# Kernel tuning notes

Hardware: AMD Instinct MI355X
Metric: run time of the kernel (lower is better)

The kernel has to match this reference:

```python
import jax, jax.numpy as jnp
import numpy as np

EPS = 1e-8  # torch.nn.CosineSimilarity default eps


def setup_inputs() -> dict:
    key = jax.random.key(0)
    k1, k2 = jax.random.split(key)
    action_set = jax.random.normal(k1, (1_000_000, 64), dtype=jnp.float32)
    pred_action = jax.random.normal(k2, (32, 4, 64), dtype=jnp.float32)
    return {"pred_action": pred_action, "action_set": action_set}


def reference(pred_action, action_set):
    # pred_action: [B, T, D] (a 2-D [B, D] input would be unsqueezed to T=1)
    # action_set:  [N, D]
    if pred_action.ndim == 2:
        pred_action = pred_action[:, None, :]
    # torch CosineSimilarity: x1.x2 / max(||x1|| * ||x2||, eps)
    dot = jnp.einsum('nd,btd->nbt', action_set, pred_action)        # [N, B, T]
    na = jnp.linalg.norm(action_set, axis=-1)                       # [N]
    nb = jnp.linalg.norm(pred_action, axis=-1)                      # [B, T]
    sims = dot / jnp.maximum(na[:, None, None] * nb[None, :, :], EPS)
    amax = jnp.argmax(sims, axis=0)                                  # [B, T]
    return action_set[amax]                                          # [B, T, D]
```

## Files before the change

### kernel.cpp

```cpp
#include <hip/hip_runtime.h>
#include <hip/hip_bf16.h>
#include <math.h>

#define D        64
#define NQ       128
#define TS       64
#define MARGIN   0.025f
#define CAP      128

typedef __attribute__((ext_vector_type(8))) short  short8;
typedef __attribute__((ext_vector_type(4))) float  f32x4;

__device__ inline unsigned ordf(float f) {
    unsigned u = __float_as_uint(f);
    return (u & 0x80000000u) ? ~u : (u | 0x80000000u);
}

__device__ inline short bf16bits(float f) {
    __hip_bfloat16 h = __float2bfloat16(f);
    return *(short*)&h;
}

__device__ inline float sq16(f32x4 a, f32x4 b, f32x4 c, f32x4 d) {
    float s = 0.f;
    s = fmaf(a.x, a.x, s); s = fmaf(a.y, a.y, s); s = fmaf(a.z, a.z, s); s = fmaf(a.w, a.w, s);
    s = fmaf(b.x, b.x, s); s = fmaf(b.y, b.y, s); s = fmaf(b.z, b.z, s); s = fmaf(b.w, b.w, s);
    s = fmaf(c.x, c.x, s); s = fmaf(c.y, c.y, s); s = fmaf(c.z, c.z, s); s = fmaf(c.w, c.w, s);
    s = fmaf(d.x, d.x, s); s = fmaf(d.y, d.y, s); s = fmaf(d.z, d.z, s); s = fmaf(d.w, d.w, s);
    return s;
}

__device__ inline short8 cvt8(f32x4 a, f32x4 b, float s) {
    short8 r;
    r[0] = bf16bits(a.x * s); r[1] = bf16bits(a.y * s);
    r[2] = bf16bits(a.z * s); r[3] = bf16bits(a.w * s);
    r[4] = bf16bits(b.x * s); r[5] = bf16bits(b.y * s);
    r[6] = bf16bits(b.z * s); r[7] = bf16bits(b.w * s);
    return r;
}

__global__ __launch_bounds__(256, 2)
void k1_score(const float* __restrict__ pred,
              const float* __restrict__ acts,
              float* __restrict__ tmax,
              int ntiles)
{
    const int tid  = threadIdx.x;
    const int lane = tid & 63;
    const int quad = lane >> 4;
    const int l15  = lane & 15;
    const int wid  = blockIdx.x * 4 + (tid >> 6);
    const int nw   = gridDim.x * 4;

    short8 bf[8][2];
#pragma unroll
    for (int nt = 0; nt < 8; ++nt) {
        const int q = nt * 16 + l15;
        const float* P = pred + q * D + quad * 8;
        f32x4 v0 = *(const f32x4*)(P);
        f32x4 v1 = *(const f32x4*)(P + 4);
        f32x4 v2 = *(const f32x4*)(P + 32);
        f32x4 v3 = *(const f32x4*)(P + 36);
        float nb2 = sq16(v0, v1, v2, v3);
        nb2 += __shfl_xor(nb2, 16);
        nb2 += __shfl_xor(nb2, 32);
        const float rnb = 1.0f / sqrtf(nb2);
        bf[nt][0] = cvt8(v0, v1, rnb);
        bf[nt][1] = cvt8(v2, v3, rnb);
    }

    for (int tile = wid; tile < ntiles; tile += nw) {
        const float* base = acts + (size_t)tile * (TS * D);

        f32x4 af[4][2][2];
#pragma unroll
        for (int mt = 0; mt < 4; ++mt) {
            const float* rp = base + (mt * 16 + l15) * D + quad * 8;
#pragma unroll
            for (int ks = 0; ks < 2; ++ks) {
                af[mt][ks][0] = *(const f32x4*)(rp + ks * 32);
                af[mt][ks][1] = *(const f32x4*)(rp + ks * 32 + 4);
            }
        }

        short8 abf[4][2];
#pragma unroll
        for (int mt = 0; mt < 4; ++mt) {
            float s = sq16(af[mt][0][0], af[mt][0][1], af[mt][1][0], af[mt][1][1]);
            s += __shfl_xor(s, 16);
            s += __shfl_xor(s, 32);
            const float r = 1.0f / sqrtf(s);
            abf[mt][0] = cvt8(af[mt][0][0], af[mt][0][1], r);
            abf[mt][1] = cvt8(af[mt][1][0], af[mt][1][1], r);
        }

#pragma unroll
        for (int nt = 0; nt < 8; ++nt) {
            f32x4 acc[4];
#pragma unroll
            for (int mt = 0; mt < 4; ++mt) acc[mt] = (f32x4){0.f, 0.f, 0.f, 0.f};
#pragma unroll
            for (int ks = 0; ks < 2; ++ks)
#pragma unroll
                for (int mt = 0; mt < 4; ++mt)
                    acc[mt] = __builtin_amdgcn_mfma_f32_16x16x32_bf16(
                        abf[mt][ks], bf[nt][ks], acc[mt], 0, 0, 0);

            float m = -3.0e38f;
#pragma unroll
            for (int mt = 0; mt < 4; ++mt) {
                m = fmaxf(m, fmaxf(fmaxf(acc[mt].x, acc[mt].y),
                                   fmaxf(acc[mt].z, acc[mt].w)));
            }
            m = fmaxf(m, __shfl_xor(m, 16));
            m = fmaxf(m, __shfl_xor(m, 32));
            if (quad == 0)
                tmax[(size_t)(nt * 16 + l15) * ntiles + tile] = m;
        }
    }
}

__global__ __launch_bounds__(256, 2)
void k2_rescore(const float* __restrict__ pred,
                const float* __restrict__ acts,
                const float* __restrict__ tmax,
                float* __restrict__ out,
                int ntiles)
{
    __shared__ float wmax[4];
    __shared__ int   cnt;
    __shared__ int   list[CAP];

    const int q   = blockIdx.x;
    const int tid = threadIdx.x;
    const float* row = tmax + (size_t)q * ntiles;

    if (tid == 0) cnt = 0;
    float m = -3.0e38f;
    for (int t = tid; t < ntiles; t += 256) m = fmaxf(m, row[t]);
#pragma unroll
    for (int off = 1; off < 64; off <<= 1) m = fmaxf(m, __shfl_xor(m, off));
    if ((tid & 63) == 0) wmax[tid >> 6] = m;
    __syncthreads();
    m = fmaxf(fmaxf(wmax[0], wmax[1]), fmaxf(wmax[2], wmax[3]));
    const float thr = m - MARGIN;

    for (int t = tid; t < ntiles; t += 256) {
        if (row[t] >= thr) {
            int i = atomicAdd(&cnt, 1);
            if (i < CAP) list[i] = t;
        }
    }
    __syncthreads();
    const int n = min(cnt, CAP);

    if (tid < 64) {
        const f32x4* P = (const f32x4*)(pred + q * D);
        unsigned long long best = 0ull;
        for (int i = 0; i < n; ++i) {
            const int r = list[i] * TS + tid;
            const f32x4* A = (const f32x4*)(acts + (size_t)r * D);
            float dot = 0.f, na2 = 0.f;
#pragma unroll
            for (int c = 0; c < 16; ++c) {
                f32x4 a = A[c];
                f32x4 p = P[c];
                dot = fmaf(a.x, p.x, dot); na2 = fmaf(a.x, a.x, na2);
                dot = fmaf(a.y, p.y, dot); na2 = fmaf(a.y, a.y, na2);
                dot = fmaf(a.z, p.z, dot); na2 = fmaf(a.z, a.z, na2);
                dot = fmaf(a.w, p.w, dot); na2 = fmaf(a.w, a.w, na2);
            }
            float sim = dot * (1.0f / sqrtf(na2));
            unsigned long long key =
                ((unsigned long long)ordf(sim) << 32) | (unsigned)(~r);
#pragma unroll
            for (int off = 1; off < 64; off <<= 1) {
                unsigned long long o = __shfl_xor(key, off);
                if (o > key) key = o;
            }
            if (key > best) best = key;
        }
        const unsigned idx = ~(unsigned)(best & 0xffffffffull);
        out[q * D + tid] = acts[(size_t)idx * D + tid];
    }
}

extern "C" void kernel_launch(void* const* d_in, const int* in_sizes, int n_in,
                              void* d_out, int out_size, void* d_ws, size_t ws_size,
                              hipStream_t stream)
{
    const float* pred = (const float*)d_in[0];
    const float* acts = (const float*)d_in[1];
    long n0 = in_sizes[0], n1 = in_sizes[1];
    if (n0 > n1) {
        const float* t = pred; pred = acts; acts = t;
        long tt = n0; n0 = n1; n1 = tt;
    }
    const int N      = (int)(n1 / D);
    const int ntiles = N / TS;

    float* tmax = (float*)d_ws;
    float* out  = (float*)d_out;

    k1_score<<<dim3(512), dim3(256), 0, stream>>>(pred, acts, tmax, ntiles);
    k2_rescore<<<dim3(NQ), dim3(256), 0, stream>>>(pred, acts, tmax, out, ntiles);
}
```

Measured before the change: 392.8 us.

## Stage action tiles in double-buffered LDS shared across waves with query split

Each block now loads a 64-row action tile cooperatively with coalesced loads, normalizes it, and converts it to bf16 into a padded, double-buffered LDS array. The four waves each handle 32 of the 128 queries against the shared tile, and the next tile's global load is prefetched while the current tile's MFMAs run. This replaces the old scheme where each wave loaded and converted its own tile and held all 128 query fragments in registers. The aim is better load coalescing, less redundant conversion and fewer registers, which allows 3 blocks per SM and a 768-block grid. The cost is a __syncthreads per tile and LDS traffic.

```diff
diff --git a/kernel.cpp b/kernel.cpp
--- a/kernel.cpp
+++ b/kernel.cpp
@@ -5,10 +5,12 @@
 #define D        64
 #define NQ       128
 #define TS       64
+#define ASTRIDE  72
 #define MARGIN   0.025f
 #define CAP      128
 
 typedef __attribute__((ext_vector_type(8))) short  short8;
+typedef __attribute__((ext_vector_type(4))) short  short4v;
 typedef __attribute__((ext_vector_type(4))) float  f32x4;
 
 __device__ inline unsigned ordf(float f) {
@@ -21,13 +23,15 @@
     return *(short*)&h;
 }
 
+__device__ inline float sq4(f32x4 a) {
+    float s = 0.f;
+    s = fmaf(a.x, a.x, s); s = fmaf(a.y, a.y, s);
+    s = fmaf(a.z, a.z, s); s = fmaf(a.w, a.w, s);
+    return s;
+}
+
 __device__ inline float sq16(f32x4 a, f32x4 b, f32x4 c, f32x4 d) {
-    float s = 0.f;
-    s = fmaf(a.x, a.x, s); s = fmaf(a.y, a.y, s); s = fmaf(a.z, a.z, s); s = fmaf(a.w, a.w, s);
-    s = fmaf(b.x, b.x, s); s = fmaf(b.y, b.y, s); s = fmaf(b.z, b.z, s); s = fmaf(b.w, b.w, s);
-    s = fmaf(c.x, c.x, s); s = fmaf(c.y, c.y, s); s = fmaf(c.z, c.z, s); s = fmaf(c.w, c.w, s);
-    s = fmaf(d.x, d.x, s); s = fmaf(d.y, d.y, s); s = fmaf(d.z, d.z, s); s = fmaf(d.w, d.w, s);
-    return s;
+    return sq4(a) + sq4(b) + sq4(c) + sq4(d);
 }
 
 __device__ inline short8 cvt8(f32x4 a, f32x4 b, float s) {
@@ -39,23 +43,31 @@
     return r;
 }
 
-__global__ __launch_bounds__(256, 2)
+__device__ inline short4v cvt4(f32x4 a, float s) {
+    short4v r;
+    r[0] = bf16bits(a.x * s); r[1] = bf16bits(a.y * s);
+    r[2] = bf16bits(a.z * s); r[3] = bf16bits(a.w * s);
+    return r;
+}
+
+__global__ __launch_bounds__(256, 3)
 void k1_score(const float* __restrict__ pred,
               const float* __restrict__ acts,
               float* __restrict__ tmax,
               int ntiles)
 {
+    __shared__ unsigned short As[2][TS * ASTRIDE];
+
     const int tid  = threadIdx.x;
     const int lane = tid & 63;
+    const int wv   = tid >> 6;
     const int quad = lane >> 4;
     const int l15  = lane & 15;
-    const int wid  = blockIdx.x * 4 + (tid >> 6);
-    const int nw   = gridDim.x * 4;
-
-    short8 bf[8][2];
-#pragma unroll
-    for (int nt = 0; nt < 8; ++nt) {
-        const int q = nt * 16 + l15;
+
+    short8 bf[2][2];
+#pragma unroll
+    for (int nt = 0; nt < 2; ++nt) {
+        const int q = (wv * 2 + nt) * 16 + l15;
         const float* P = pred + q * D + quad * 8;
         f32x4 v0 = *(const f32x4*)(P);
         f32x4 v1 = *(const f32x4*)(P + 4);
@@ -69,54 +81,89 @@
         bf[nt][1] = cvt8(v2, v3, rnb);
     }
 
-    for (int tile = wid; tile < ntiles; tile += nw) {
-        const float* base = acts + (size_t)tile * (TS * D);
-
-        f32x4 af[4][2][2];
-#pragma unroll
-        for (int mt = 0; mt < 4; ++mt) {
-            const float* rp = base + (mt * 16 + l15) * D + quad * 8;
-#pragma unroll
-            for (int ks = 0; ks < 2; ++ks) {
-                af[mt][ks][0] = *(const f32x4*)(rp + ks * 32);
-                af[mt][ks][1] = *(const f32x4*)(rp + ks * 32 + 4);
-            }
-        }
-
-        short8 abf[4][2];
-#pragma unroll
-        for (int mt = 0; mt < 4; ++mt) {
-            float s = sq16(af[mt][0][0], af[mt][0][1], af[mt][1][0], af[mt][1][1]);
-            s += __shfl_xor(s, 16);
-            s += __shfl_xor(s, 32);
-            const float r = 1.0f / sqrtf(s);
-            abf[mt][0] = cvt8(af[mt][0][0], af[mt][0][1], r);
-            abf[mt][1] = cvt8(af[mt][1][0], af[mt][1][1], r);
-        }
-
-#pragma unroll
-        for (int nt = 0; nt < 8; ++nt) {
-            f32x4 acc[4];
-#pragma unroll
-            for (int mt = 0; mt < 4; ++mt) acc[mt] = (f32x4){0.f, 0.f, 0.f, 0.f};
+    int tile = blockIdx.x;
+    if (tile >= ntiles) return;
+
+    {
+        const f32x4* src = (const f32x4*)(acts + (size_t)tile * (TS * D));
+        f32x4 v[4];
+#pragma unroll
+        for (int i = 0; i < 4; ++i) v[i] = src[tid + i * 256];
+#pragma unroll
+        for (int i = 0; i < 4; ++i) {
+            const int c   = tid + i * 256;
+            const int row = c >> 4, col = c & 15;
+            float s = sq4(v[i]);
+            s += __shfl_xor(s, 1); s += __shfl_xor(s, 2);
+            s += __shfl_xor(s, 4); s += __shfl_xor(s, 8);
+            *(short4v*)&As[0][row * ASTRIDE + col * 4] = cvt4(v[i], 1.0f / sqrtf(s));
+        }
+    }
+    __syncthreads();
+
+    int p = 0;
+    while (true) {
+        const int tn = tile + gridDim.x;
+        const bool have_next = tn < ntiles;
+
+        f32x4 v[4];
+        if (have_next) {
+            const f32x4* src = (const f32x4*)(acts + (size_t)tn * (TS * D));
+#pragma unroll
+            for (int i = 0; i < 4; ++i) v[i] = src[tid + i * 256];
+        }
+
+        short8 af[4][2];
+#pragma unroll
+        for (int mt = 0; mt < 4; ++mt)
 #pragma unroll
             for (int ks = 0; ks < 2; ++ks)
+                af[mt][ks] = *(const short8*)
+                    &As[p][(mt * 16 + l15) * ASTRIDE + ks * 32 + quad * 8];
+
+        f32x4 acc[2][4];
+#pragma unroll
+        for (int nt = 0; nt < 2; ++nt)
+#pragma unroll
+            for (int mt = 0; mt < 4; ++mt) acc[nt][mt] = (f32x4){0.f, 0.f, 0.f, 0.f};
+#pragma unroll
+        for (int ks = 0; ks < 2; ++ks)
+#pragma unroll
+            for (int nt = 0; nt < 2; ++nt)
 #pragma unroll
                 for (int mt = 0; mt < 4; ++mt)
-                    acc[mt] = __builtin_amdgcn_mfma_f32_16x16x32_bf16(
-                        abf[mt][ks], bf[nt][ks], acc[mt], 0, 0, 0);
-
+                    acc[nt][mt] = __builtin_amdgcn_mfma_f32_16x16x32_bf16(
+                        af[mt][ks], bf[nt][ks], acc[nt][mt], 0, 0, 0);
+
+#pragma unroll
+        for (int nt = 0; nt < 2; ++nt) {
             float m = -3.0e38f;
 #pragma unroll
-            for (int mt = 0; mt < 4; ++mt) {
-                m = fmaxf(m, fmaxf(fmaxf(acc[mt].x, acc[mt].y),
-                                   fmaxf(acc[mt].z, acc[mt].w)));
-            }
+            for (int mt = 0; mt < 4; ++mt)
+                m = fmaxf(m, fmaxf(fmaxf(acc[nt][mt].x, acc[nt][mt].y),
+                                   fmaxf(acc[nt][mt].z, acc[nt][mt].w)));
             m = fmaxf(m, __shfl_xor(m, 16));
             m = fmaxf(m, __shfl_xor(m, 32));
-            if (quad == 0)
-                tmax[(size_t)(nt * 16 + l15) * ntiles + tile] = m;
-        }
+            if (quad == 0) {
+                const int q = (wv * 2 + nt) * 16 + l15;
+                tmax[(size_t)q * ntiles + tile] = m;
+            }
+        }
+
+        if (!have_next) break;
+
+#pragma unroll
+        for (int i = 0; i < 4; ++i) {
+            const int c   = tid + i * 256;
+            const int row = c >> 4, col = c & 15;
+            float s = sq4(v[i]);
+            s += __shfl_xor(s, 1); s += __shfl_xor(s, 2);
+            s += __shfl_xor(s, 4); s += __shfl_xor(s, 8);
+            *(short4v*)&As[p ^ 1][row * ASTRIDE + col * 4] = cvt4(v[i], 1.0f / sqrtf(s));
+        }
+        __syncthreads();
+        p ^= 1;
+        tile = tn;
     }
 }
 
@@ -164,11 +211,11 @@
 #pragma unroll
             for (int c = 0; c < 16; ++c) {
                 f32x4 a = A[c];
-                f32x4 p = P[c];
-                dot = fmaf(a.x, p.x, dot); na2 = fmaf(a.x, a.x, na2);
-                dot = fmaf(a.y, p.y, dot); na2 = fmaf(a.y, a.y, na2);
-                dot = fmaf(a.z, p.z, dot); na2 = fmaf(a.z, a.z, na2);
-                dot = fmaf(a.w, p.w, dot); na2 = fmaf(a.w, a.w, na2);
+                f32x4 pq = P[c];
+                dot = fmaf(a.x, pq.x, dot); na2 = fmaf(a.x, a.x, na2);
+                dot = fmaf(a.y, pq.y, dot); na2 = fmaf(a.y, a.y, na2);
+                dot = fmaf(a.z, pq.z, dot); na2 = fmaf(a.z, a.z, na2);
+                dot = fmaf(a.w, pq.w, dot); na2 = fmaf(a.w, a.w, na2);
             }
             float sim = dot * (1.0f / sqrtf(na2));
             unsigned long long key =
@@ -202,6 +249,6 @@
     float* tmax = (float*)d_ws;
     float* out  = (float*)d_out;
 
-    k1_score<<<dim3(512), dim3(256), 0, stream>>>(pred, acts, tmax, ntiles);
+    k1_score<<<dim3(768), dim3(256), 0, stream>>>(pred, acts, tmax, ntiles);
     k2_rescore<<<dim3(NQ), dim3(256), 0, stream>>>(pred, acts, tmax, out, ntiles);
 }
```

New measurement: 383.7 us. 2.3% less time.
